# Kernel tuning notes

Measured on AMD Instinct MI355X. Metric: run time of the kernel, lower is better.

## Reference

```python
import jax, jax.numpy as jnp
import numpy as np

G = 64        # graphs per batch
NPG = 1024    # nodes per graph (static)
DEG = 8       # avg degree
INF = 128
HID = 256
OUT = 256
N = G * NPG
E = N * DEG
K1 = 512      # ceil(0.5 * 1024)
K2 = 256      # ceil(0.5 * 512)
EPS = 1e-5


def setup_inputs() -> dict:
    key = jax.random.key(0)
    ks = jax.random.split(key, 12)
    s = 0.05
    x = jax.random.normal(ks[0], (N, INF), jnp.float32)
    off = (jnp.arange(G, dtype=jnp.int32) * NPG)[:, None]
    src = (jax.random.randint(ks[1], (G, NPG * DEG), 0, NPG, jnp.int32) + off).reshape(-1)
    dst = (jax.random.randint(ks[2], (G, NPG * DEG), 0, NPG, jnp.int32) + off).reshape(-1)
    return {
        'x': x, 'src': src, 'dst': dst,
        'W_rel1': jax.random.normal(ks[3], (INF, HID), jnp.float32) * s,
        'b_rel1': jnp.zeros((HID,), jnp.float32),
        'W_root1': jax.random.normal(ks[4], (INF, HID), jnp.float32) * s,
        'g1': jnp.ones((HID,), jnp.float32), 'bt1': jnp.zeros((HID,), jnp.float32),
        'p1': jax.random.normal(ks[5], (HID,), jnp.float32) * s,
        'g2': jnp.ones((HID,), jnp.float32), 'bt2': jnp.zeros((HID,), jnp.float32),
        'W_rel2': jax.random.normal(ks[6], (HID, HID), jnp.float32) * s,
        'b_rel2': jnp.zeros((HID,), jnp.float32),
        'W_root2': jax.random.normal(ks[7], (HID, HID), jnp.float32) * s,
        'p2': jax.random.normal(ks[8], (HID,), jnp.float32) * s,
        'Wl': jax.random.normal(ks[9], (2 * HID, OUT), jnp.float32) * s,
        'bl': jnp.zeros((OUT,), jnp.float32),
    }


def _bn(x, g, b):
    # training-mode BatchNorm over nodes (biased variance), as nn.BatchNorm1d
    m = x.mean(0)
    v = x.var(0)
    return (x - m) * jax.lax.rsqrt(v + EPS) * g + b


def _conv(x, src, dst, emask, W_rel, b_rel, W_root):
    # GraphConv: sum_{j->i} x_j, then lin_rel(aggr) + lin_root(x)
    msg = x[src]                                    # [E, F] gather
    if emask is not None:
        msg = jnp.where(emask[:, None], msg, 0.0)   # dropped edges contribute 0
    agg = jax.ops.segment_sum(msg, dst, num_segments=x.shape[0])
    return agg @ W_rel + b_rel + x @ W_root


def _pool(x, src, dst, emask, p, n, k):
    # TopKPooling: score = tanh((x.p)/||p||); keep top-k per graph; x *= score
    score = jnp.tanh((x @ p) / jnp.linalg.norm(p))  # [G*n]
    vals, idx = jax.lax.top_k(score.reshape(G, n), k)   # [G, k] per-graph
    perm = (idx + (jnp.arange(G, dtype=jnp.int32) * n)[:, None]).reshape(-1)
    xn = x[perm] * vals.reshape(-1)[:, None]        # [G*k, F]
    # remap old node ids -> new ids; -1 marks dropped nodes
    mapping = jnp.full((G * n,), -1, jnp.int32).at[perm].set(
        jnp.arange(G * k, dtype=jnp.int32))
    ns, nd = mapping[src], mapping[dst]
    nmask = emask & (ns >= 0) & (nd >= 0)
    ns = jnp.where(nmask, ns, 0)
    nd = jnp.where(nmask, nd, 0)
    return xn, ns, nd, nmask


def reference(x, src, dst, W_rel1, b_rel1, W_root1, g1, bt1, p1,
              g2, bt2, W_rel2, b_rel2, W_root2, p2, Wl, bl):
    act = lambda v: jax.nn.gelu(v, approximate=False)
    h = _conv(x, src, dst, None, W_rel1, b_rel1, W_root1)
    h = _bn(act(h), g1, bt1)
    h, s1, d1, m1 = _pool(h, src, dst, jnp.ones((E,), bool), p1, NPG, K1)
    hg = h.reshape(G, K1, HID)
    x1 = jnp.concatenate([hg.max(1), hg.mean(1)], axis=1)   # [G, 2H] gmp|gap
    h = act(_bn(h, g2, bt2))
    h = _conv(h, s1, d1, m1, W_rel2, b_rel2, W_root2)
    h, s2, d2, m2 = _pool(h, s1, d1, m1, p2, K1, K2)
    hg = h.reshape(G, K2, HID)
    x2 = jnp.concatenate([hg.max(1), hg.mean(1)], axis=1)
    return (x1 + x2) @ Wl + bl                              # [G, OUT]
```

## Files before the change

### kernel.cpp

```cpp
#include <hip/hip_runtime.h>
#include <hip/hip_bf16.h>
#include <float.h>

#define GG    64
#define NPG   1024
#define EPG   8192
#define NE    524288
#define FIN   128
#define HID   256
#define K1    512
#define K2    256
#define NN0   65536
#define NN1   32768
#define NN2   16384
#define EPSBN 1e-5f

typedef _Float16 f16x8 __attribute__((ext_vector_type(8)));
typedef _Float16 f16x4 __attribute__((ext_vector_type(4)));
typedef float f32x4 __attribute__((ext_vector_type(4)));

__device__ __forceinline__ float gelu_exact(float v) {
    return 0.5f * v * (1.0f + erff(v * 0.7071067811865476f));
}

__device__ __forceinline__ void gld16(const void* g, void* lds) {
    __builtin_amdgcn_global_load_lds(
        (const __attribute__((address_space(1))) unsigned int*)g,
        (__attribute__((address_space(3))) unsigned int*)lds, 16, 0, 0);
}

__global__ __launch_bounds__(512) void k_prepcsr(
        const int* __restrict__ src, const int* __restrict__ dst,
        int* __restrict__ rowp, int* __restrict__ ssrc, int* __restrict__ map1,
        const float* __restrict__ Wrel1, const float* __restrict__ Wroot1,
        const float* __restrict__ Wrel2, const float* __restrict__ Wroot2,
        const float* __restrict__ p2,
        _Float16* __restrict__ W1h, _Float16* __restrict__ W2h,
        float* __restrict__ q2, float* __restrict__ stats1,
        float* __restrict__ stats2) {
    __shared__ int cnt[NPG];
    __shared__ int sa[NPG];
    __shared__ int sb[NPG];
    __shared__ float red[256];
    const int b = blockIdx.x, tid = threadIdx.x;
    if (b < 64) {
        const int g = b;
        const int eb = g * EPG;
        for (int i = g * 512 + tid; i < NN0; i += GG * 512) map1[i] = -1;
        for (int i = tid; i < NPG; i += 512) cnt[i] = 0;
        __syncthreads();
        for (int e = tid; e < EPG; e += 512)
            atomicAdd(&cnt[dst[eb + e] & (NPG - 1)], 1);
        __syncthreads();
        for (int i = tid; i < NPG; i += 512) sa[i] = cnt[i];
        __syncthreads();
        int* cur = sa; int* nxt = sb;
        for (int d = 1; d < NPG; d <<= 1) {
            for (int i = tid; i < NPG; i += 512)
                nxt[i] = cur[i] + ((i >= d) ? cur[i - d] : 0);
            __syncthreads();
            int* t = cur; cur = nxt; nxt = t;
        }
        for (int i = tid; i < NPG; i += 512) {
            const int st = cur[i] - cnt[i];
            rowp[g * (NPG + 1) + i] = st;
            cnt[i] = st;
        }
        if (tid == 0) rowp[g * (NPG + 1) + NPG] = EPG;
        __syncthreads();
        for (int e = tid; e < EPG; e += 512) {
            const int d = dst[eb + e] & (NPG - 1);
            const int p = atomicAdd(&cnt[d], 1);
            ssrc[eb + p] = src[eb + e] & (NPG - 1);
        }
    } else if (b < 192) {
        const int i = (b - 64) * 512 + tid;
        const int n = i >> 8, k = i & 255;
        const float v = (k < FIN) ? Wrel1[k * HID + n] : Wroot1[(k - FIN) * HID + n];
        W1h[i] = (_Float16)v;
    } else if (b < 448) {
        const int i = (b - 192) * 512 + tid;
        const int n = i >> 9, k = i & 511;
        const float v = (k < HID) ? Wrel2[k * HID + n] : Wroot2[(k - HID) * HID + n];
        W2h[i] = (_Float16)v;
    } else if (b == 448) {
        if (tid < 256) { const float pv = p2[tid]; red[tid] = pv * pv; }
        __syncthreads();
        for (int s = 128; s > 0; s >>= 1) {
            if (tid < s) red[tid] += red[tid + s];
            __syncthreads();
        }
        if (tid < 256) q2[tid] = p2[tid] * rsqrtf(red[0]);
    } else {
        stats1[tid] = 0.f;
        stats2[tid] = 0.f;
    }
}

__global__ __launch_bounds__(256) void k_agg1(const float* __restrict__ x,
        const int* __restrict__ rowp, const int* __restrict__ ssrc,
        _Float16* __restrict__ A1) {
    const int b = blockIdx.x;
    const int g = b & 63;
    const int ng = b >> 6;
    const int tid = threadIdx.x;
    const int ln = tid & 31;
    const int node = (ng << 3) + (tid >> 5);
    const int s0 = rowp[g * (NPG + 1) + node];
    const int s1 = rowp[g * (NPG + 1) + node + 1];
    const float4* x4 = reinterpret_cast<const float4*>(x);
    const size_t gb = (size_t)(g << 10) * 32;
    const int* sp = ssrc + (size_t)g * EPG;
    float4 acc = make_float4(0.f, 0.f, 0.f, 0.f);
    for (int j = s0; j < s1; ++j) {
        const float4 v = x4[gb + (size_t)sp[j] * 32 + ln];
        acc.x += v.x; acc.y += v.y; acc.z += v.z; acc.w += v.w;
    }
    const size_t rb = ((size_t)((g << 10) + node)) * 256;
    *reinterpret_cast<f16x4*>(&A1[rb + (ln << 2)]) =
        (f16x4){(_Float16)acc.x, (_Float16)acc.y, (_Float16)acc.z, (_Float16)acc.w};
    const float4 xv = x4[gb + (size_t)node * 32 + ln];
    *reinterpret_cast<f16x4*>(&A1[rb + 128 + (ln << 2)]) =
        (f16x4){(_Float16)xv.x, (_Float16)xv.y, (_Float16)xv.z, (_Float16)xv.w};
}

__global__ __launch_bounds__(256) void k_agg2(const _Float16* __restrict__ A2r,
        const int* __restrict__ rowp, const int* __restrict__ ssrc,
        const int* __restrict__ perm1, const int* __restrict__ map1,
        _Float16* __restrict__ A2w) {
    const int b = blockIdx.x;
    const int g = b & 63;
    const int ng = b >> 6;
    const int tid = threadIdx.x;
    const int ln = tid & 63;
    const int ni = (ng << 2) + (tid >> 6);
    const int on = perm1[(g << 9) + ni] & (NPG - 1);
    const int s0 = rowp[g * (NPG + 1) + on];
    const int s1 = rowp[g * (NPG + 1) + on + 1];
    const int* sp = ssrc + (size_t)g * EPG;
    const int* mp = map1 + ((size_t)g << 10);
    float4 acc = make_float4(0.f, 0.f, 0.f, 0.f);
    for (int j = s0; j < s1; ++j) {
        const int ms = mp[sp[j]];
        if (ms < 0) continue;
        const f16x4 v = *reinterpret_cast<const f16x4*>(
            &A2r[(size_t)ms * 512 + 256 + (ln << 2)]);
        acc.x += (float)v[0]; acc.y += (float)v[1];
        acc.z += (float)v[2]; acc.w += (float)v[3];
    }
    *reinterpret_cast<f16x4*>(&A2w[((size_t)((g << 9) + ni)) * 512 + (ln << 2)]) =
        (f16x4){(_Float16)acc.x, (_Float16)acc.y, (_Float16)acc.z, (_Float16)acc.w};
}

template<int K, int EPI>
__global__ __launch_bounds__(512, 4) void k_gemm(
        const _Float16* __restrict__ A, const _Float16* __restrict__ B,
        const float* __restrict__ bias, _Float16* __restrict__ C,
        float* __restrict__ stats, const float* __restrict__ qv2,
        float* __restrict__ scores, int M) {
    __shared__ _Float16 Ash[3][128 * 32];
    __shared__ _Float16 Bsh[3][256 * 32];
    __shared__ float csum[256];
    __shared__ float csq[256];
    const int tid = threadIdx.x;
    const int l = tid & 63, w = tid >> 6;
    const int wm = w >> 2, wn = w & 3;
    const int m0 = blockIdx.x * 128;
    const int r16 = l & 15, kg = l >> 4;

    const int srA = (w << 4) + (l >> 2);
    const int swA = ((l & 3) ^ ((srA >> 1) & 3)) << 3;
    const size_t aoff = (size_t)(m0 + srA) * K + swA;
    const int ldsA = w << 10;
    const int srB0 = (w << 5) + (l >> 2);
    const int srB1 = srB0 + 16;
    const int swB0 = ((l & 3) ^ ((srB0 >> 1) & 3)) << 3;
    const int swB1 = ((l & 3) ^ ((srB1 >> 1) & 3)) << 3;
    const size_t boff0 = (size_t)srB0 * K + swB0;
    const size_t boff1 = (size_t)srB1 * K + swB1;
    const int ldsB0 = w << 11, ldsB1 = (w << 11) + 1024;

    f32x4 acc[4][4] = {};
    constexpr int NI = K / 32;

    gld16(A + aoff,       (char*)Ash[0] + ldsA);
    gld16(B + boff0,      (char*)Bsh[0] + ldsB0);
    gld16(B + boff1,      (char*)Bsh[0] + ldsB1);
    gld16(A + aoff + 32,  (char*)Ash[1] + ldsA);
    gld16(B + boff0 + 32, (char*)Bsh[1] + ldsB0);
    gld16(B + boff1 + 32, (char*)Bsh[1] + ldsB1);

#pragma unroll
    for (int i = 0; i < NI; ++i) {
        const int k0 = i * 32;
        const int cur = i % 3;
        __builtin_amdgcn_s_barrier();
        if (i + 2 < NI) {
            const int nxt = (i + 2) % 3;
            gld16(A + aoff + k0 + 64,  (char*)Ash[nxt] + ldsA);
            gld16(B + boff0 + k0 + 64, (char*)Bsh[nxt] + ldsB0);
            gld16(B + boff1 + k0 + 64, (char*)Bsh[nxt] + ldsB1);
            asm volatile("s_waitcnt vmcnt(6)" ::: "memory");
        } else if (i + 1 < NI) {
            asm volatile("s_waitcnt vmcnt(3)" ::: "memory");
        } else {
            asm volatile("s_waitcnt vmcnt(0)" ::: "memory");
        }
        __builtin_amdgcn_s_barrier();
        __builtin_amdgcn_sched_barrier(0);
        const char* ab = (const char*)Ash[cur];
        const char* bb = (const char*)Bsh[cur];
        f16x8 af[4], bf[4];
#pragma unroll
        for (int mi = 0; mi < 4; ++mi) {
            const int r = wm * 64 + mi * 16 + r16;
            const int bo = r * 64 + ((kg ^ ((r >> 1) & 3)) << 4);
            af[mi] = *reinterpret_cast<const f16x8*>(ab + bo);
        }
#pragma unroll
        for (int ni = 0; ni < 4; ++ni) {
            const int r = wn * 64 + ni * 16 + r16;
            const int bo = r * 64 + ((kg ^ ((r >> 1) & 3)) << 4);
            bf[ni] = *reinterpret_cast<const f16x8*>(bb + bo);
        }
#pragma unroll
        for (int mi = 0; mi < 4; ++mi)
#pragma unroll
            for (int ni = 0; ni < 4; ++ni)
                acc[mi][ni] = __builtin_amdgcn_mfma_f32_16x16x32_f16(
                    af[mi], bf[ni], acc[mi][ni], 0, 0, 0);
    }

    if (EPI == 1) {
        if (tid < 256) { csum[tid] = 0.f; csq[tid] = 0.f; }
        __syncthreads();
    }

    float qv[4];
    if (EPI == 2) {
#pragma unroll
        for (int ni = 0; ni < 4; ++ni) qv[ni] = qv2[wn * 64 + ni * 16 + r16];
    }
    float sA[4] = {0, 0, 0, 0};
    float qA[4] = {0, 0, 0, 0};
    float sp[4][4] = {};
#pragma unroll
    for (int mi = 0; mi < 4; ++mi)
#pragma unroll
        for (int ni = 0; ni < 4; ++ni) {
            const int col = wn * 64 + ni * 16 + r16;
            const float bc = bias[col];
#pragma unroll
            for (int r = 0; r < 4; ++r) {
                const int row = m0 + wm * 64 + mi * 16 + (kg << 2) + r;
                float t = acc[mi][ni][r] + bc;
                if (EPI == 1) {
                    t = gelu_exact(t);
                    sA[ni] += t;
                    qA[ni] += t * t;
                }
                if (EPI == 2) sp[mi][r] += t * qv[ni];
                C[(size_t)row * 256 + col] = (_Float16)t;
            }
        }
    if (EPI == 1) {
#pragma unroll
        for (int ni = 0; ni < 4; ++ni) {
            const int cl = wn * 64 + ni * 16 + r16;
            unsafeAtomicAdd(&csum[cl], sA[ni]);
            unsafeAtomicAdd(&csq[cl], qA[ni]);
        }
        __syncthreads();
        if (tid < 256) {
            unsafeAtomicAdd(&stats[tid], csum[tid]);
            unsafeAtomicAdd(&stats[HID + tid], csq[tid]);
        }
    }
    if (EPI == 2) {
        const int slot = wn;
#pragma unroll
        for (int mi = 0; mi < 4; ++mi)
#pragma unroll
            for (int r = 0; r < 4; ++r) {
                float s = sp[mi][r];
                s += __shfl_xor(s, 1);
                s += __shfl_xor(s, 2);
                s += __shfl_xor(s, 4);
                s += __shfl_xor(s, 8);
                if (r16 == 0)
                    scores[(size_t)slot * M + m0 + wm * 64 + mi * 16 + (kg << 2) + r] = s;
            }
    }
}

__global__ __launch_bounds__(256) void k_finalize1(const float* __restrict__ stats,
        const float* __restrict__ g1, const float* __restrict__ bt1,
        const float* __restrict__ p1, float* __restrict__ scale,
        float* __restrict__ shift, float* __restrict__ q, float* __restrict__ r) {
    __shared__ float red[256];
    const int c = threadIdx.x;
    const float m = stats[c] * (1.f / NN0);
    const float v = stats[HID + c] * (1.f / NN0) - m * m;
    const float sc = g1[c] * rsqrtf(v + EPSBN);
    const float sh = bt1[c] - m * sc;
    scale[c] = sc;
    shift[c] = sh;
    const float pv = p1[c];
    red[c] = pv * pv;
    __syncthreads();
    for (int s = 128; s > 0; s >>= 1) {
        if (c < s) red[c] += red[c + s];
        __syncthreads();
    }
    const float inv = rsqrtf(red[0]);
    q[c] = sc * pv * inv;
    __syncthreads();
    red[c] = sh * pv * inv;
    __syncthreads();
    for (int s = 128; s > 0; s >>= 1) {
        if (c < s) red[c] += red[c + s];
        __syncthreads();
    }
    if (c == 0) r[0] = red[0];
}

__global__ __launch_bounds__(256) void k_finalize2(const float* __restrict__ stats,
        const float* __restrict__ g2, const float* __restrict__ bt2,
        float* __restrict__ scale, float* __restrict__ shift) {
    const int c = threadIdx.x;
    const float m = stats[c] * (1.f / NN1);
    const float v = stats[HID + c] * (1.f / NN1) - m * m;
    const float sc = g2[c] * rsqrtf(v + EPSBN);
    scale[c] = sc;
    shift[c] = bt2[c] - m * sc;
}

__global__ __launch_bounds__(256) void k_score(const _Float16* __restrict__ H,
        const float* __restrict__ q, const float* __restrict__ r,
        float* __restrict__ out) {
    const int node = blockIdx.x * 4 + (threadIdx.x >> 6);
    const int lane = threadIdx.x & 63;
    const f16x4 h = *reinterpret_cast<const f16x4*>(H + (size_t)node * HID + (lane << 2));
    const float4 qv = *reinterpret_cast<const float4*>(q + (lane << 2));
    float d = (float)h[0] * qv.x + (float)h[1] * qv.y +
              (float)h[2] * qv.z + (float)h[3] * qv.w;
#pragma unroll
    for (int off = 32; off > 0; off >>= 1) d += __shfl_xor(d, off);
    if (lane == 0) out[node] = d + (r ? r[0] : 0.f);
}

template<int NN_, int KK_, int NT_>
__global__ __launch_bounds__(NT_) void k_topk(const float* __restrict__ scores,
        int nparts, int pstride, int* __restrict__ perm,
        float* __restrict__ vals, int* __restrict__ mapping) {
    __shared__ float s[NN_];
    __shared__ int id[NN_];
    const int g = blockIdx.x, tid = threadIdx.x;
    for (int i = tid; i < NN_; i += NT_) {
        float raw = 0.f;
        for (int p = 0; p < nparts; ++p)
            raw += scores[(size_t)p * pstride + g * NN_ + i];
        s[i] = tanhf(raw);
        id[i] = i;
    }
    __syncthreads();
    for (int k = 2; k <= NN_; k <<= 1) {
        for (int j = k >> 1; j > 0; j >>= 1) {
            for (int t = tid; t < NN_; t += NT_) {
                const int ixj = t ^ j;
                if (ixj > t) {
                    const bool desc = ((t & k) == 0);
                    const float s1 = s[t], s2 = s[ixj];
                    const int i1 = id[t], i2 = id[ixj];
                    const bool inOrder = (s1 > s2) || (s1 == s2 && i1 < i2);
                    if (inOrder != desc) { s[t] = s2; s[ixj] = s1; id[t] = i2; id[ixj] = i1; }
                }
            }
            __syncthreads();
        }
    }
    for (int i = tid; i < KK_; i += NT_) {
        const int oid = id[i];
        perm[g * KK_ + i] = g * NN_ + oid;
        vals[g * KK_ + i] = s[i];
        if (mapping) mapping[g * NN_ + oid] = g * KK_ + i;
    }
}

__global__ __launch_bounds__(256) void k_pool1p(const _Float16* __restrict__ HG,
        const int* __restrict__ perm, const float* __restrict__ vals,
        const float* __restrict__ scale1, const float* __restrict__ shift1,
        float* __restrict__ pmax, float* __restrict__ psum,
        float* __restrict__ psq) {
    const int b = blockIdx.x;
    const int g = b >> 3, ig = b & 7;
    const int c = threadIdx.x;
    const float sc = scale1[c], sh = shift1[c];
    float mx = -FLT_MAX, sm = 0.f, sq = 0.f;
    for (int i = ig * 64; i < ig * 64 + 64; ++i) {
        const int idx = (g << 9) + i;
        const int srow = perm[idx];
        const float val = vals[idx];
        const float hv = (float)HG[(size_t)srow * HID + c];
        const float xn = (hv * sc + sh) * val;
        mx = fmaxf(mx, xn);
        sm += xn;
        sq += xn * xn;
    }
    pmax[b * 256 + c] = mx;
    psum[b * 256 + c] = sm;
    psq[b * 256 + c] = sq;
}

__global__ __launch_bounds__(256) void k_pool1r(const float* __restrict__ pmax,
        const float* __restrict__ psum, const float* __restrict__ psq,
        float* __restrict__ X1, float* __restrict__ stats2) {
    const int g = blockIdx.x, c = threadIdx.x;
    float mx = -FLT_MAX, sm = 0.f, sq = 0.f;
    for (int ig = 0; ig < 8; ++ig) {
        const int o = ((g << 3) + ig) * 256 + c;
        mx = fmaxf(mx, pmax[o]);
        sm += psum[o];
        sq += psq[o];
    }
    X1[g * 512 + c] = mx;
    X1[g * 512 + 256 + c] = sm * (1.f / K1);
    unsafeAtomicAdd(&stats2[c], sm);
    unsafeAtomicAdd(&stats2[HID + c], sq);
}

__global__ __launch_bounds__(256) void k_h2in(const _Float16* __restrict__ HG,
        const int* __restrict__ perm, const float* __restrict__ vals,
        const float* __restrict__ scale1, const float* __restrict__ shift1,
        const float* __restrict__ scale2, const float* __restrict__ shift2,
        _Float16* __restrict__ A2) {
    const int i = blockIdx.x * 256 + threadIdx.x;
    const int idx = i >> 6, c4 = i & 63;
    const int srow = perm[idx];
    const float val = vals[idx];
    const f16x4 h = *reinterpret_cast<const f16x4*>(&HG[(size_t)srow * HID + (c4 << 2)]);
    const float4 s1 = reinterpret_cast<const float4*>(scale1)[c4];
    const float4 b1 = reinterpret_cast<const float4*>(shift1)[c4];
    const float4 s2 = reinterpret_cast<const float4*>(scale2)[c4];
    const float4 b2 = reinterpret_cast<const float4*>(shift2)[c4];
    const float x0 = ((float)h[0] * s1.x + b1.x) * val;
    const float x1 = ((float)h[1] * s1.y + b1.y) * val;
    const float x2 = ((float)h[2] * s1.z + b1.z) * val;
    const float x3 = ((float)h[3] * s1.w + b1.w) * val;
    *reinterpret_cast<f16x4*>(&A2[(size_t)idx * 512 + 256 + (c4 << 2)]) =
        (f16x4){(_Float16)gelu_exact(x0 * s2.x + b2.x),
                (_Float16)gelu_exact(x1 * s2.y + b2.y),
                (_Float16)gelu_exact(x2 * s2.z + b2.z),
                (_Float16)gelu_exact(x3 * s2.w + b2.w)};
}

__global__ __launch_bounds__(256) void k_x2p(const _Float16* __restrict__ H2,
        const int* __restrict__ perm, const float* __restrict__ vals,
        float* __restrict__ pmax, float* __restrict__ psum) {
    const int b = blockIdx.x;
    const int g = b >> 3, ig = b & 7;
    const int c = threadIdx.x;
    float mx = -FLT_MAX, sm = 0.f;
    for (int i = ig * 32; i < ig * 32 + 32; ++i) {
        const int idx = (g << 8) + i;
        const int srow = perm[idx];
        const float v = (float)H2[(size_t)srow * HID + c] * vals[idx];
        mx = fmaxf(mx, v);
        sm += v;
    }
    pmax[b * 256 + c] = mx;
    psum[b * 256 + c] = sm;
}

__global__ __launch_bounds__(256) void k_x2final(const float* __restrict__ pmax,
        const float* __restrict__ psum, const float* __restrict__ X1,
        const float* __restrict__ Wl, const float* __restrict__ bl,
        float* __restrict__ out) {
    __shared__ float sx2[512];
    const int g = blockIdx.x, c = threadIdx.x;
    float mx = -FLT_MAX, sm = 0.f;
    for (int ig = 0; ig < 8; ++ig) {
        const int o = ((g << 3) + ig) * 256 + c;
        mx = fmaxf(mx, pmax[o]);
        sm += psum[o];
    }
    sx2[c] = mx;
    sx2[256 + c] = sm * (1.f / K2);
    __syncthreads();
    float acc = bl[c];
    for (int k = 0; k < 512; ++k) {
        const float xv = X1[g * 512 + k] + sx2[k];
        acc = fmaf(xv, Wl[k * HID + c], acc);
    }
    out[g * HID + c] = acc;
}

extern "C" void kernel_launch(void* const* d_in, const int* in_sizes, int n_in,
                              void* d_out, int out_size, void* d_ws, size_t ws_size,
                              hipStream_t stream) {
    (void)in_sizes; (void)n_in; (void)out_size; (void)ws_size;
    const float* x       = (const float*)d_in[0];
    const int*   src     = (const int*)  d_in[1];
    const int*   dst     = (const int*)  d_in[2];
    const float* W_rel1  = (const float*)d_in[3];
    const float* b_rel1  = (const float*)d_in[4];
    const float* W_root1 = (const float*)d_in[5];
    const float* g1      = (const float*)d_in[6];
    const float* bt1     = (const float*)d_in[7];
    const float* p1      = (const float*)d_in[8];
    const float* g2      = (const float*)d_in[9];
    const float* bt2     = (const float*)d_in[10];
    const float* W_rel2  = (const float*)d_in[11];
    const float* b_rel2  = (const float*)d_in[12];
    const float* W_root2 = (const float*)d_in[13];
    const float* p2      = (const float*)d_in[14];
    const float* Wl      = (const float*)d_in[15];
    const float* bl      = (const float*)d_in[16];
    float* out = (float*)d_out;

    char* w = (char*)d_ws;
    size_t off = 0;
    auto alloc = [&](size_t bytes) -> void* {
        void* p = w + off;
        off += (bytes + 255) & ~(size_t)255;
        return p;
    };
    _Float16* A1  = (_Float16*)alloc((size_t)NN0 * 256 * 2);
    _Float16* HG  = (_Float16*)alloc((size_t)NN0 * 256 * 2);
    _Float16* H2  = (_Float16*)alloc((size_t)NN1 * 256 * 2);
    int*   ROWP   = (int*)  alloc((size_t)GG * (NPG + 1) * 4);
    int*   SSRC   = (int*)  alloc((size_t)NE * 4);
    float* SCORES = (float*)alloc((size_t)4 * NN1 * 4);
    int*   PERM1  = (int*)  alloc((size_t)NN1 * 4);
    float* VALS1  = (float*)alloc((size_t)NN1 * 4);
    int*   MAP1   = (int*)  alloc((size_t)NN0 * 4);
    int*   PERM2  = (int*)  alloc((size_t)NN2 * 4);
    float* VALS2  = (float*)alloc((size_t)NN2 * 4);
    float* STATS1 = (float*)alloc(512 * 4);
    float* STATS2 = (float*)alloc(512 * 4);
    float* SCALE1 = (float*)alloc(256 * 4);
    float* SHIFT1 = (float*)alloc(256 * 4);
    float* Q1     = (float*)alloc(256 * 4);
    float* R1     = (float*)alloc(256);
    float* SCALE2 = (float*)alloc(256 * 4);
    float* SHIFT2 = (float*)alloc(256 * 4);
    float* Q2     = (float*)alloc(256 * 4);
    _Float16* W1h = (_Float16*)alloc((size_t)256 * 256 * 2);
    _Float16* W2h = (_Float16*)alloc((size_t)256 * 512 * 2);
    float* X1     = (float*)alloc((size_t)GG * 512 * 4);
    float* PMAX   = (float*)alloc((size_t)512 * 256 * 4);
    float* PSUM   = (float*)alloc((size_t)512 * 256 * 4);
    float* PSQ    = (float*)alloc((size_t)512 * 256 * 4);
    _Float16* A2 = A1;

    k_prepcsr<<<450, 512, 0, stream>>>(src, dst, ROWP, SSRC, MAP1,
        W_rel1, W_root1, W_rel2, W_root2, p2, W1h, W2h, Q2, STATS1, STATS2);
    k_agg1<<<8192, 256, 0, stream>>>(x, ROWP, SSRC, A1);
    k_gemm<256, 1><<<512, 512, 0, stream>>>(A1, W1h, b_rel1, HG, STATS1,
        nullptr, nullptr, NN0);
    k_finalize1<<<1, 256, 0, stream>>>(STATS1, g1, bt1, p1, SCALE1, SHIFT1, Q1, R1);
    k_score<<<NN0 / 4, 256, 0, stream>>>(HG, Q1, R1, SCORES);
    k_topk<NPG, K1, 512><<<GG, 512, 0, stream>>>(SCORES, 1, 0, PERM1, VALS1, MAP1);
    k_pool1p<<<512, 256, 0, stream>>>(HG, PERM1, VALS1, SCALE1, SHIFT1, PMAX, PSUM, PSQ);
    k_pool1r<<<GG, 256, 0, stream>>>(PMAX, PSUM, PSQ, X1, STATS2);
    k_finalize2<<<1, 256, 0, stream>>>(STATS2, g2, bt2, SCALE2, SHIFT2);
    k_h2in<<<8192, 256, 0, stream>>>(HG, PERM1, VALS1, SCALE1, SHIFT1,
        SCALE2, SHIFT2, A2);
    k_agg2<<<8192, 256, 0, stream>>>(A2, ROWP, SSRC, PERM1, MAP1, A2);
    k_gemm<512, 2><<<256, 512, 0, stream>>>(A2, W2h, b_rel2, H2, nullptr,
        Q2, SCORES, NN1);
    k_topk<K1, K2, 256><<<GG, 256, 0, stream>>>(SCORES, 4, NN1, PERM2, VALS2, nullptr);
    k_x2p<<<512, 256, 0, stream>>>(H2, PERM2, VALS2, PMAX, PSUM);
    k_x2final<<<GG, 256, 0, stream>>>(PMAX, PSUM, X1, Wl, bl, out);
}
```

Baseline: 257.6 us.

## Restructure GEMM to keep full weight tile in LDS, stream A from global

```diff
diff --git a/kernel.cpp b/kernel.cpp
--- a/kernel.cpp
+++ b/kernel.cpp
@@ -152,124 +152,99 @@
         (f16x4){(_Float16)acc.x, (_Float16)acc.y, (_Float16)acc.z, (_Float16)acc.w};
 }
 
-template<int K, int EPI>
-__global__ __launch_bounds__(512, 4) void k_gemm(
+template<int K, int EPI, int MCH>
+__global__ __launch_bounds__(512, 2) void k_gemmB(
         const _Float16* __restrict__ A, const _Float16* __restrict__ B,
         const float* __restrict__ bias, _Float16* __restrict__ C,
         float* __restrict__ stats, const float* __restrict__ qv2,
         float* __restrict__ scores, int M) {
-    __shared__ _Float16 Ash[3][128 * 32];
-    __shared__ _Float16 Bsh[3][256 * 32];
+    __shared__ _Float16 Bs[256 * 256];
     __shared__ float csum[256];
     __shared__ float csq[256];
     const int tid = threadIdx.x;
     const int l = tid & 63, w = tid >> 6;
-    const int wm = w >> 2, wn = w & 3;
-    const int m0 = blockIdx.x * 128;
+    constexpr int BM = 8 * MCH * 16;
+    const int m0 = blockIdx.x * BM;
     const int r16 = l & 15, kg = l >> 4;
 
-    const int srA = (w << 4) + (l >> 2);
-    const int swA = ((l & 3) ^ ((srA >> 1) & 3)) << 3;
-    const size_t aoff = (size_t)(m0 + srA) * K + swA;
-    const int ldsA = w << 10;
-    const int srB0 = (w << 5) + (l >> 2);
-    const int srB1 = srB0 + 16;
-    const int swB0 = ((l & 3) ^ ((srB0 >> 1) & 3)) << 3;
-    const int swB1 = ((l & 3) ^ ((srB1 >> 1) & 3)) << 3;
-    const size_t boff0 = (size_t)srB0 * K + swB0;
-    const size_t boff1 = (size_t)srB1 * K + swB1;
-    const int ldsB0 = w << 11, ldsB1 = (w << 11) + 1024;
-
-    f32x4 acc[4][4] = {};
-    constexpr int NI = K / 32;
-
-    gld16(A + aoff,       (char*)Ash[0] + ldsA);
-    gld16(B + boff0,      (char*)Bsh[0] + ldsB0);
-    gld16(B + boff1,      (char*)Bsh[0] + ldsB1);
-    gld16(A + aoff + 32,  (char*)Ash[1] + ldsA);
-    gld16(B + boff0 + 32, (char*)Bsh[1] + ldsB0);
-    gld16(B + boff1 + 32, (char*)Bsh[1] + ldsB1);
-
-#pragma unroll
-    for (int i = 0; i < NI; ++i) {
-        const int k0 = i * 32;
-        const int cur = i % 3;
-        __builtin_amdgcn_s_barrier();
-        if (i + 2 < NI) {
-            const int nxt = (i + 2) % 3;
-            gld16(A + aoff + k0 + 64,  (char*)Ash[nxt] + ldsA);
-            gld16(B + boff0 + k0 + 64, (char*)Bsh[nxt] + ldsB0);
-            gld16(B + boff1 + k0 + 64, (char*)Bsh[nxt] + ldsB1);
-            asm volatile("s_waitcnt vmcnt(6)" ::: "memory");
-        } else if (i + 1 < NI) {
-            asm volatile("s_waitcnt vmcnt(3)" ::: "memory");
-        } else {
-            asm volatile("s_waitcnt vmcnt(0)" ::: "memory");
-        }
-        __builtin_amdgcn_s_barrier();
-        __builtin_amdgcn_sched_barrier(0);
-        const char* ab = (const char*)Ash[cur];
-        const char* bb = (const char*)Bsh[cur];
-        f16x8 af[4], bf[4];
-#pragma unroll
-        for (int mi = 0; mi < 4; ++mi) {
-            const int r = wm * 64 + mi * 16 + r16;
-            const int bo = r * 64 + ((kg ^ ((r >> 1) & 3)) << 4);
-            af[mi] = *reinterpret_cast<const f16x8*>(ab + bo);
-        }
-#pragma unroll
-        for (int ni = 0; ni < 4; ++ni) {
-            const int r = wn * 64 + ni * 16 + r16;
-            const int bo = r * 64 + ((kg ^ ((r >> 1) & 3)) << 4);
-            bf[ni] = *reinterpret_cast<const f16x8*>(bb + bo);
-        }
-#pragma unroll
-        for (int mi = 0; mi < 4; ++mi)
-#pragma unroll
-            for (int ni = 0; ni < 4; ++ni)
-                acc[mi][ni] = __builtin_amdgcn_mfma_f32_16x16x32_f16(
-                    af[mi], bf[ni], acc[mi][ni], 0, 0, 0);
+    f32x4 acc[MCH][16] = {};
+    constexpr int PH = K / 256;
+
+#pragma unroll
+    for (int ph = 0; ph < PH; ++ph) {
+        if (ph) __syncthreads();
+        for (int u = tid; u < 8192; u += 512) {
+            const int row = u >> 5, slot = u & 31;
+            const int gch = slot ^ (row & 7);
+            gld16(B + (size_t)row * K + ph * 256 + gch * 8, (char*)Bs + u * 16);
+        }
+        asm volatile("s_waitcnt vmcnt(0)" ::: "memory");
+        __syncthreads();
+
+#pragma unroll
+        for (int ks = 0; ks < 8; ++ks) {
+            f16x8 a[MCH];
+#pragma unroll
+            for (int mc = 0; mc < MCH; ++mc) {
+                const int mrow = m0 + (w * MCH + mc) * 16 + r16;
+                a[mc] = *reinterpret_cast<const f16x8*>(
+                    A + (size_t)mrow * K + ph * 256 + ks * 32 + kg * 8);
+            }
+#pragma unroll
+            for (int ni = 0; ni < 16; ++ni) {
+                const int brow = ni * 16 + r16;
+                const int c = ks * 4 + kg;
+                const int pos = c ^ (brow & 7);
+                const f16x8 bf = *reinterpret_cast<const f16x8*>(
+                    (const char*)Bs + (brow * 32 + pos) * 16);
+#pragma unroll
+                for (int mc = 0; mc < MCH; ++mc)
+                    acc[mc][ni] = __builtin_amdgcn_mfma_f32_16x16x32_f16(
+                        a[mc], bf, acc[mc][ni], 0, 0, 0);
+            }
+        }
     }
 
     if (EPI == 1) {
+        __syncthreads();
         if (tid < 256) { csum[tid] = 0.f; csq[tid] = 0.f; }
         __syncthreads();
     }
 
-    float qv[4];
+    float sp[MCH][4];
     if (EPI == 2) {
 #pragma unroll
-        for (int ni = 0; ni < 4; ++ni) qv[ni] = qv2[wn * 64 + ni * 16 + r16];
-    }
-    float sA[4] = {0, 0, 0, 0};
-    float qA[4] = {0, 0, 0, 0};
-    float sp[4][4] = {};
-#pragma unroll
-    for (int mi = 0; mi < 4; ++mi)
-#pragma unroll
-        for (int ni = 0; ni < 4; ++ni) {
-            const int col = wn * 64 + ni * 16 + r16;
-            const float bc = bias[col];
+        for (int mc = 0; mc < MCH; ++mc)
+#pragma unroll
+            for (int r = 0; r < 4; ++r) sp[mc][r] = 0.f;
+    }
+#pragma unroll
+    for (int ni = 0; ni < 16; ++ni) {
+        const int col = ni * 16 + r16;
+        const float bc = bias[col];
+        const float qvn = (EPI == 2) ? qv2[col] : 0.f;
+        float sA = 0.f, qA = 0.f;
+#pragma unroll
+        for (int mc = 0; mc < MCH; ++mc) {
 #pragma unroll
             for (int r = 0; r < 4; ++r) {
-                const int row = m0 + wm * 64 + mi * 16 + (kg << 2) + r;
-                float t = acc[mi][ni][r] + bc;
+                const int row = m0 + (w * MCH + mc) * 16 + (kg << 2) + r;
+                float t = acc[mc][ni][r] + bc;
                 if (EPI == 1) {
                     t = gelu_exact(t);
-                    sA[ni] += t;
-                    qA[ni] += t * t;
+                    sA += t;
+                    qA += t * t;
                 }
-                if (EPI == 2) sp[mi][r] += t * qv[ni];
+                if (EPI == 2) sp[mc][r] += t * qvn;
                 C[(size_t)row * 256 + col] = (_Float16)t;
             }
         }
+        if (EPI == 1) {
+            unsafeAtomicAdd(&csum[col], sA);
+            unsafeAtomicAdd(&csq[col], qA);
+        }
+    }
     if (EPI == 1) {
-#pragma unroll
-        for (int ni = 0; ni < 4; ++ni) {
-            const int cl = wn * 64 + ni * 16 + r16;
-            unsafeAtomicAdd(&csum[cl], sA[ni]);
-            unsafeAtomicAdd(&csq[cl], qA[ni]);
-        }
         __syncthreads();
         if (tid < 256) {
             unsafeAtomicAdd(&stats[tid], csum[tid]);
@@ -277,18 +252,17 @@
         }
     }
     if (EPI == 2) {
-        const int slot = wn;
-#pragma unroll
-        for (int mi = 0; mi < 4; ++mi)
+#pragma unroll
+        for (int mc = 0; mc < MCH; ++mc)
 #pragma unroll
             for (int r = 0; r < 4; ++r) {
-                float s = sp[mi][r];
+                float s = sp[mc][r];
                 s += __shfl_xor(s, 1);
                 s += __shfl_xor(s, 2);
                 s += __shfl_xor(s, 4);
                 s += __shfl_xor(s, 8);
                 if (r16 == 0)
-                    scores[(size_t)slot * M + m0 + wm * 64 + mi * 16 + (kg << 2) + r] = s;
+                    scores[m0 + (w * MCH + mc) * 16 + (kg << 2) + r] = s;
             }
     }
 }
@@ -530,7 +504,7 @@
     _Float16* H2  = (_Float16*)alloc((size_t)NN1 * 256 * 2);
     int*   ROWP   = (int*)  alloc((size_t)GG * (NPG + 1) * 4);
     int*   SSRC   = (int*)  alloc((size_t)NE * 4);
-    float* SCORES = (float*)alloc((size_t)4 * NN1 * 4);
+    float* SCORES = (float*)alloc((size_t)NN0 * 4);
     int*   PERM1  = (int*)  alloc((size_t)NN1 * 4);
     float* VALS1  = (float*)alloc((size_t)NN1 * 4);
     int*   MAP1   = (int*)  alloc((size_t)NN0 * 4);
@@ -556,7 +530,7 @@
     k_prepcsr<<<450, 512, 0, stream>>>(src, dst, ROWP, SSRC, MAP1,
         W_rel1, W_root1, W_rel2, W_root2, p2, W1h, W2h, Q2, STATS1, STATS2);
     k_agg1<<<8192, 256, 0, stream>>>(x, ROWP, SSRC, A1);
-    k_gemm<256, 1><<<512, 512, 0, stream>>>(A1, W1h, b_rel1, HG, STATS1,
+    k_gemmB<256, 1, 2><<<256, 512, 0, stream>>>(A1, W1h, b_rel1, HG, STATS1,
         nullptr, nullptr, NN0);
     k_finalize1<<<1, 256, 0, stream>>>(STATS1, g1, bt1, p1, SCALE1, SHIFT1, Q1, R1);
     k_score<<<NN0 / 4, 256, 0, stream>>>(HG, Q1, R1, SCORES);
@@ -567,9 +541,9 @@
     k_h2in<<<8192, 256, 0, stream>>>(HG, PERM1, VALS1, SCALE1, SHIFT1,
         SCALE2, SHIFT2, A2);
     k_agg2<<<8192, 256, 0, stream>>>(A2, ROWP, SSRC, PERM1, MAP1, A2);
-    k_gemm<512, 2><<<256, 512, 0, stream>>>(A2, W2h, b_rel2, H2, nullptr,
+    k_gemmB<512, 2, 1><<<256, 512, 0, stream>>>(A2, W2h, b_rel2, H2, nullptr,
         Q2, SCORES, NN1);
-    k_topk<K1, K2, 256><<<GG, 256, 0, stream>>>(SCORES, 4, NN1, PERM2, VALS2, nullptr);
+    k_topk<K1, K2, 256><<<GG, 256, 0, stream>>>(SCORES, 1, 0, PERM2, VALS2, nullptr);
     k_x2p<<<512, 256, 0, stream>>>(H2, PERM2, VALS2, PMAX, PSUM);
     k_x2final<<<GG, 256, 0, stream>>>(PMAX, PSUM, X1, Wl, bl, out);
 }
```

Result: no change. 253.0 us (-1.8%).
